# Performance work log

Hardware: AMD Instinct MI355X
Metric: run time of the kernel (lower is better)

The kernel has to match this reference:

```python
import jax, jax.numpy as jnp
import numpy as np

N_USERS = 50000
N_ENTITIES = 100000
N_NODES = N_USERS + N_ENTITIES
N_EDGES = 3000000
EMB_DIM = 64
WEIGHT_SIZES = [64, 64, 32, 16]  # [emb_dim] + weight_size
BATCH = 8192
LEAKY_SLOPE = 0.2  # KGAT (TF reference) uses leaky_relu alpha=0.2
EPS = 1e-12


def setup_inputs() -> dict:
    key = jax.random.key(0)
    ks = jax.random.split(key, 24)
    inp = {}
    inp["users"] = jax.random.randint(ks[0], (BATCH,), 0, N_USERS, dtype=jnp.int32)
    inp["pos_items"] = jax.random.randint(ks[1], (BATCH,), 0, N_ENTITIES, dtype=jnp.int32)
    inp["neg_items"] = jax.random.randint(ks[2], (BATCH,), 0, N_ENTITIES, dtype=jnp.int32)
    inp["all_h"] = jax.random.randint(ks[3], (N_EDGES,), 0, N_NODES, dtype=jnp.int32)
    inp["all_t"] = jax.random.randint(ks[4], (N_EDGES,), 0, N_NODES, dtype=jnp.int32)
    inp["A_values"] = jax.random.uniform(ks[5], (N_EDGES,), dtype=jnp.float32)
    inp["user_embed"] = jax.random.normal(ks[6], (N_USERS, EMB_DIM), dtype=jnp.float32) * 0.1
    inp["entity_embed"] = jax.random.normal(ks[7], (N_ENTITIES, EMB_DIM), dtype=jnp.float32) * 0.1
    ki = 8
    for k in range(3):
        din, dout = WEIGHT_SIZES[k], WEIGHT_SIZES[k + 1]
        scale = float(np.sqrt(2.0 / (din + dout)))  # xavier-ish
        inp[f"W_gc_{k}"] = jax.random.normal(ks[ki], (din, dout), dtype=jnp.float32) * scale; ki += 1
        inp[f"b_gc_{k}"] = jax.random.normal(ks[ki], (1, dout), dtype=jnp.float32) * scale; ki += 1
        inp[f"W_bi_{k}"] = jax.random.normal(ks[ki], (din, dout), dtype=jnp.float32) * scale; ki += 1
        inp[f"b_bi_{k}"] = jax.random.normal(ks[ki], (1, dout), dtype=jnp.float32) * scale; ki += 1
    return inp


def _bi_interaction(ego, all_h, all_t, A_values, layers, n_nodes):
    # KGAT bi-interaction aggregator over edge-list sparse adjacency.
    outs = [ego]
    for (W_gc, b_gc, W_bi, b_bi) in layers:
        # sparse A @ ego : gather tails, weight by attention, scatter-add to heads
        msgs = A_values[:, None] * ego[all_t]                       # [E, d]
        side = jax.ops.segment_sum(msgs, all_h, num_segments=n_nodes)  # [N, d]
        sum_emb = jax.nn.leaky_relu((ego + side) @ W_gc + b_gc, negative_slope=LEAKY_SLOPE)
        bi_emb = jax.nn.leaky_relu((ego * side) @ W_bi + b_bi, negative_slope=LEAKY_SLOPE)
        ego = sum_emb + bi_emb
        norm = ego / jnp.maximum(jnp.linalg.norm(ego, axis=1, keepdims=True), EPS)
        outs.append(norm)
    return jnp.concatenate(outs, axis=1)  # [N, 64+64+32+16]


def reference(users, pos_items, neg_items, all_h, all_t, A_values,
              user_embed, entity_embed,
              W_gc_0, b_gc_0, W_bi_0, b_bi_0,
              W_gc_1, b_gc_1, W_bi_1, b_bi_1,
              W_gc_2, b_gc_2, W_bi_2, b_bi_2):
    n_users = user_embed.shape[0]
    n_nodes = n_users + entity_embed.shape[0]
    ego = jnp.concatenate([user_embed, entity_embed], axis=0)  # [N, 64]
    layers = [(W_gc_0, b_gc_0, W_bi_0, b_bi_0),
              (W_gc_1, b_gc_1, W_bi_1, b_bi_1),
              (W_gc_2, b_gc_2, W_bi_2, b_bi_2)]
    all_emb = _bi_interaction(ego, all_h, all_t, A_values, layers, n_nodes)
    ua, ea = all_emb[:n_users], all_emb[n_users:]
    u_e = ua[users]
    pos_i_e = ea[pos_items]
    neg_i_e = ea[neg_items]
    return (u_e, pos_i_e, neg_i_e)
```

## Files before the change

### kernel.cpp

```cpp
#include <hip/hip_runtime.h>
#include <math.h>

#define N_USERS    50000
#define N_ENTITIES 100000
#define N_NODES    150000
#define N_EDGES    3000000
#define BATCH      8192
#define SLOPE      0.2f
#define EPSF       1e-12f

#define NBUK   2344
#define CAP    1536
#define STR    2560
#define PADM   16
#define BLK_E  12288
#define NPB    ((N_EDGES + BLK_E - 1) / BLK_E)
#define PBLK   1024
#define EPT    (BLK_E / PBLK)
#define CH     4096
#define GC_STRIDE 16
#define CASTB  ((N_NODES * 64 / 4 + PBLK - 1) / PBLK)

__device__ __forceinline__ unsigned f2bf(float f) {
    unsigned u = __float_as_uint(f);
    return (u + 0x7FFFu + ((u >> 16) & 1u)) >> 16;
}
__device__ __forceinline__ float bf_lo(unsigned d) { return __uint_as_float(d << 16); }
__device__ __forceinline__ float bf_hi(unsigned d) { return __uint_as_float(d); }

__global__ __launch_bounds__(PBLK)
void prep_k(const int* __restrict__ all_h, const int* __restrict__ all_t,
            const float* __restrict__ A,
            int* __restrict__ gcursor, int2* __restrict__ rec,
            const float* __restrict__ user_emb, const float* __restrict__ ent_emb,
            unsigned short* __restrict__ ego0_bf) {
    __shared__ int pos[NBUK];
    __shared__ int gofs[NBUK];
    __shared__ int wsum[PBLK / 64];
    __shared__ int2 srec[CH];
    __shared__ int  sdst[CH];

    int t = threadIdx.x;

    if (blockIdx.x >= NPB) {
        int idx = (blockIdx.x - NPB) * PBLK + t;
        const int total = N_NODES * 64 / 4;
        if (idx >= total) return;
        int ge = idx * 4;
        const float* src = (ge < N_USERS * 64) ? user_emb + ge
                                               : ent_emb + (ge - N_USERS * 64);
        float4 v = *(const float4*)src;
        ushort4 o;
        o.x = (unsigned short)f2bf(v.x);
        o.y = (unsigned short)f2bf(v.y);
        o.z = (unsigned short)f2bf(v.z);
        o.w = (unsigned short)f2bf(v.w);
        *(ushort4*)(ego0_bf + ge) = o;
        return;
    }

    for (int i = t; i < NBUK; i += PBLK) pos[i] = 0;
    __syncthreads();

    int e0 = blockIdx.x * BLK_E;
    int e1 = e0 + BLK_E; if (e1 > N_EDGES) e1 = N_EDGES;
    int tot = e1 - e0;

    int h[EPT]; int tt[EPT]; float aa[EPT];
    #pragma unroll
    for (int k = 0; k < EPT; ++k) {
        int e = e0 + k * PBLK + t;
        bool v = e < e1;
        h[k]  = v ? all_h[e] : -1;
        tt[k] = v ? all_t[e] : 0;
        aa[k] = v ? A[e] : 0.f;
    }
    #pragma unroll
    for (int k = 0; k < EPT; ++k)
        if (h[k] >= 0) atomicAdd(&pos[h[k] >> 6], 1);
    __syncthreads();

    int c[3], g[3];
    int i0 = t * 3;
    int tsum = 0;
    #pragma unroll
    for (int j = 0; j < 3; ++j) {
        int idx = i0 + j;
        c[j] = (idx < NBUK) ? pos[idx] : 0;
        tsum += c[j];
        g[j] = (idx < NBUK && c[j]) ? atomicAdd(&gcursor[idx * GC_STRIDE], c[j]) : 0;
    }

    int lane = t & 63, w = t >> 6;
    int incl = tsum;
    #pragma unroll
    for (int off = 1; off < 64; off <<= 1) {
        int x = __shfl_up(incl, off, 64);
        if (lane >= off) incl += x;
    }
    if (lane == 63) wsum[w] = incl;
    __syncthreads();
    int wbase = 0;
    for (int j = 0; j < w; ++j) wbase += wsum[j];
    int excl = wbase + (incl - tsum);

    #pragma unroll
    for (int j = 0; j < 3; ++j) {
        int idx = i0 + j;
        if (idx < NBUK) { pos[idx] = excl; gofs[idx] = g[j] - excl; }
        excl += c[j];
    }
    __syncthreads();

    int pp[EPT], gd[EPT];
    #pragma unroll
    for (int k = 0; k < EPT; ++k) {
        if (h[k] >= 0) {
            int b = h[k] >> 6;
            int p = atomicAdd(&pos[b], 1);
            pp[k] = p;
            int gr = gofs[b] + p;
            gd[k] = (gr < CAP) ? b * STR + gr : -1;
        } else {
            pp[k] = -1; gd[k] = -1;
        }
    }

    for (int base = 0; base < tot; base += CH) {
        __syncthreads();
        int lim = tot - base; if (lim > CH) lim = CH;
        #pragma unroll
        for (int k = 0; k < EPT; ++k) {
            int s = pp[k] - base;
            if (s >= 0 && s < CH) {
                srec[s] = make_int2(tt[k] | ((h[k] & 63) << 18), __float_as_int(aa[k]));
                sdst[s] = gd[k];
            }
        }
        __syncthreads();
        for (int s = t; s < lim; s += PBLK) {
            int d = sdst[s];
            if (d >= 0) rec[d] = srec[s];
        }
    }
}

__global__ __launch_bounds__(256)
void local_sort_k(const int* __restrict__ gcursor, int2* __restrict__ rec,
                  int2* __restrict__ range) {
    __shared__ int2 sin[CAP];
    __shared__ int2 sout[STR];
    __shared__ int cnt64[64];
    __shared__ int pos64[64];
    __shared__ int s_ptot;
    int b = blockIdx.x, t = threadIdx.x;
    int cnt = gcursor[(size_t)b * GC_STRIDE]; if (cnt > CAP) cnt = CAP;

    if (t < 64) cnt64[t] = 0;
    __syncthreads();

    for (int i = t; i < cnt; i += 256) {
        int2 p = rec[(size_t)b * STR + i];
        sin[i] = p;
        atomicAdd(&cnt64[(p.x >> 18) & 63], 1);
    }
    __syncthreads();

    if (t < 64) {
        int v = cnt64[t];
        int pv = (v + PADM - 1) & ~(PADM - 1);
        int sum = pv;
        #pragma unroll
        for (int off = 1; off < 64; off <<= 1) {
            int x = __shfl_up(sum, off, 64);
            if (t >= off) sum += x;
        }
        pos64[t] = sum - pv;
        if (t == 63) s_ptot = sum;
    }
    __syncthreads();
    int ptot = s_ptot;

    for (int i = t; i < ptot; i += 256) sout[i] = make_int2(0, 0);
    __syncthreads();

    for (int i = t; i < cnt; i += 256) {
        int2 p = sin[i];
        int l = (p.x >> 18) & 63;
        int dst = atomicAdd(&pos64[l], 1);
        sout[dst] = make_int2(p.x & 0x3FFFF, p.y);
    }
    __syncthreads();

    for (int i = t; i < ptot; i += 256)
        rec[(size_t)b * STR + i] = sout[i];

    if (t < 64) {
        int v = cnt64[t];
        int pv = (v + PADM - 1) & ~(PADM - 1);
        int sum = pv;
        #pragma unroll
        for (int off = 1; off < 64; off <<= 1) {
            int x = __shfl_up(sum, off, 64);
            if (t >= off) sum += x;
        }
        int start = b * STR + (sum - pv);
        int node = b * 64 + t;
        if (node < N_NODES) range[node] = make_int2(start, start + pv);
    }
}

template<int DIN>
__global__ __launch_bounds__(256)
void side_k(const int2* __restrict__ range, const int2* __restrict__ rec,
            const unsigned short* __restrict__ tab, float* __restrict__ side) {
    constexpr int LPR = DIN / 8;
    constexpr int EPW = 64 / LPR;

    int w = threadIdx.x >> 6;
    int lane = threadIdx.x & 63;
    int h = blockIdx.x * 4 + w;

    int2 rg = range[h];
    int e0 = rg.x, e1 = rg.y;
    int g = lane / LPR;
    int q = lane % LPR;

    float acc[8];
    #pragma unroll
    for (int j = 0; j < 8; ++j) acc[j] = 0.f;

    int e = e0;
    for (; e + 2 * EPW <= e1; e += 2 * EPW) {
        int2 p0 = rec[e + g];
        int2 p1 = rec[e + EPW + g];
        float a0 = __int_as_float(p0.y);
        float a1 = __int_as_float(p1.y);
        uint4 d0 = *(const uint4*)(tab + (unsigned)(p0.x * DIN) + q * 8);
        uint4 d1 = *(const uint4*)(tab + (unsigned)(p1.x * DIN) + q * 8);
        acc[0] = fmaf(a0, bf_lo(d0.x), acc[0]);
        acc[1] = fmaf(a0, bf_hi(d0.x), acc[1]);
        acc[2] = fmaf(a0, bf_lo(d0.y), acc[2]);
        acc[3] = fmaf(a0, bf_hi(d0.y), acc[3]);
        acc[4] = fmaf(a0, bf_lo(d0.z), acc[4]);
        acc[5] = fmaf(a0, bf_hi(d0.z), acc[5]);
        acc[6] = fmaf(a0, bf_lo(d0.w), acc[6]);
        acc[7] = fmaf(a0, bf_hi(d0.w), acc[7]);
        acc[0] = fmaf(a1, bf_lo(d1.x), acc[0]);
        acc[1] = fmaf(a1, bf_hi(d1.x), acc[1]);
        acc[2] = fmaf(a1, bf_lo(d1.y), acc[2]);
        acc[3] = fmaf(a1, bf_hi(d1.y), acc[3]);
        acc[4] = fmaf(a1, bf_lo(d1.z), acc[4]);
        acc[5] = fmaf(a1, bf_hi(d1.z), acc[5]);
        acc[6] = fmaf(a1, bf_lo(d1.w), acc[6]);
        acc[7] = fmaf(a1, bf_hi(d1.w), acc[7]);
    }
    if (e < e1) {
        int2 p0 = rec[e + g];
        float a0 = __int_as_float(p0.y);
        uint4 d0 = *(const uint4*)(tab + (unsigned)(p0.x * DIN) + q * 8);
        acc[0] = fmaf(a0, bf_lo(d0.x), acc[0]);
        acc[1] = fmaf(a0, bf_hi(d0.x), acc[1]);
        acc[2] = fmaf(a0, bf_lo(d0.y), acc[2]);
        acc[3] = fmaf(a0, bf_hi(d0.y), acc[3]);
        acc[4] = fmaf(a0, bf_lo(d0.z), acc[4]);
        acc[5] = fmaf(a0, bf_hi(d0.z), acc[5]);
        acc[6] = fmaf(a0, bf_lo(d0.w), acc[6]);
        acc[7] = fmaf(a0, bf_hi(d0.w), acc[7]);
    }

    #pragma unroll
    for (int off = LPR; off < 64; off <<= 1)
        #pragma unroll
        for (int j = 0; j < 8; ++j) acc[j] += __shfl_xor(acc[j], off, 64);

    if (lane < LPR) {
        float* dst = side + (size_t)h * DIN + q * 8;
        *(float4*)dst       = make_float4(acc[0], acc[1], acc[2], acc[3]);
        *(float4*)(dst + 4) = make_float4(acc[4], acc[5], acc[6], acc[7]);
    }
}

template<int DIN, int DOUT, int TILE_ROWS, bool CONCAT, bool OUT_BF>
__global__ __launch_bounds__(256)
void transform_k(const unsigned short* __restrict__ ego_in,
                 const float* __restrict__ user_emb, const float* __restrict__ ent_emb,
                 const float* __restrict__ side,
                 const float* __restrict__ Wgc, const float* __restrict__ bgc,
                 const float* __restrict__ Wbi, const float* __restrict__ bbi,
                 void* __restrict__ ego_out) {
    constexpr int NG = DOUT / 8;
    constexpr int RG = 256 / NG;
    constexpr int RT = TILE_ROWS / RG;
    constexpr int STRIDE = DIN + 4;
    constexpr int KC8 = DIN / 8;

    __shared__ float sWgc[DIN * DOUT], sWbi[DIN * DOUT];
    __shared__ float sU[TILE_ROWS * STRIDE], sV[TILE_ROWS * STRIDE];

    int t = threadIdx.x;

    for (int i = t * 4; i < DIN * DOUT; i += 1024) {
        *(float4*)&sWgc[i] = *(const float4*)&Wgc[i];
        *(float4*)&sWbi[i] = *(const float4*)&Wbi[i];
    }

    int base = blockIdx.x * TILE_ROWS;
    for (int f = t; f < TILE_ROWS * KC8; f += 256) {
        int row = f / KC8, c8 = f % KC8;
        int n = base + row;
        int nc = n < N_NODES ? n : N_NODES - 1;
        float ev[8];
        if (CONCAT) {
            const float* erow = (nc < N_USERS) ? user_emb + (size_t)nc * 64
                                               : ent_emb + (size_t)(nc - N_USERS) * 64;
            float4 a = *(const float4*)(erow + c8 * 8);
            float4 b = *(const float4*)(erow + c8 * 8 + 4);
            ev[0] = a.x; ev[1] = a.y; ev[2] = a.z; ev[3] = a.w;
            ev[4] = b.x; ev[5] = b.y; ev[6] = b.z; ev[7] = b.w;
        } else {
            uint4 d = *(const uint4*)(ego_in + (size_t)nc * DIN + c8 * 8);
            ev[0] = bf_lo(d.x); ev[1] = bf_hi(d.x);
            ev[2] = bf_lo(d.y); ev[3] = bf_hi(d.y);
            ev[4] = bf_lo(d.z); ev[5] = bf_hi(d.z);
            ev[6] = bf_lo(d.w); ev[7] = bf_hi(d.w);
        }
        const float* srow = side + (size_t)nc * DIN + c8 * 8;
        float4 s0 = *(const float4*)srow;
        float4 s1 = *(const float4*)(srow + 4);
        float sv8[8] = {s0.x, s0.y, s0.z, s0.w, s1.x, s1.y, s1.z, s1.w};
        float* pu = &sU[row * STRIDE + c8 * 8];
        float* pv = &sV[row * STRIDE + c8 * 8];
        *(float4*)pu       = make_float4(ev[0] + sv8[0], ev[1] + sv8[1], ev[2] + sv8[2], ev[3] + sv8[3]);
        *(float4*)(pu + 4) = make_float4(ev[4] + sv8[4], ev[5] + sv8[5], ev[6] + sv8[6], ev[7] + sv8[7]);
        *(float4*)pv       = make_float4(ev[0] * sv8[0], ev[1] * sv8[1], ev[2] * sv8[2], ev[3] * sv8[3]);
        *(float4*)(pv + 4) = make_float4(ev[4] * sv8[4], ev[5] * sv8[5], ev[6] * sv8[6], ev[7] * sv8[7]);
    }
    __syncthreads();

    int cg = t % NG, rgi = t / NG;
    int c0 = cg * 8;
    int r0 = rgi * RT;

    float accg[RT][8], accb[RT][8];
    #pragma unroll
    for (int r = 0; r < RT; ++r)
        #pragma unroll
        for (int j = 0; j < 8; ++j) { accg[r][j] = 0.f; accb[r][j] = 0.f; }

    for (int k = 0; k < DIN; k += 4) {
        float4 u4[RT], v4[RT];
        #pragma unroll
        for (int r = 0; r < RT; ++r) {
            u4[r] = *(const float4*)&sU[(r0 + r) * STRIDE + k];
            v4[r] = *(const float4*)&sV[(r0 + r) * STRIDE + k];
        }
        #pragma unroll
        for (int kk = 0; kk < 4; ++kk) {
            float4 wg0 = *(const float4*)&sWgc[(k + kk) * DOUT + c0];
            float4 wg1 = *(const float4*)&sWgc[(k + kk) * DOUT + c0 + 4];
            float4 wb0 = *(const float4*)&sWbi[(k + kk) * DOUT + c0];
            float4 wb1 = *(const float4*)&sWbi[(k + kk) * DOUT + c0 + 4];
            #pragma unroll
            for (int r = 0; r < RT; ++r) {
                float u = ((const float*)&u4[r])[kk];
                float v = ((const float*)&v4[r])[kk];
                accg[r][0] = fmaf(u, wg0.x, accg[r][0]);
                accg[r][1] = fmaf(u, wg0.y, accg[r][1]);
                accg[r][2] = fmaf(u, wg0.z, accg[r][2]);
                accg[r][3] = fmaf(u, wg0.w, accg[r][3]);
                accg[r][4] = fmaf(u, wg1.x, accg[r][4]);
                accg[r][5] = fmaf(u, wg1.y, accg[r][5]);
                accg[r][6] = fmaf(u, wg1.z, accg[r][6]);
                accg[r][7] = fmaf(u, wg1.w, accg[r][7]);
                accb[r][0] = fmaf(v, wb0.x, accb[r][0]);
                accb[r][1] = fmaf(v, wb0.y, accb[r][1]);
                accb[r][2] = fmaf(v, wb0.z, accb[r][2]);
                accb[r][3] = fmaf(v, wb0.w, accb[r][3]);
                accb[r][4] = fmaf(v, wb1.x, accb[r][4]);
                accb[r][5] = fmaf(v, wb1.y, accb[r][5]);
                accb[r][6] = fmaf(v, wb1.z, accb[r][6]);
                accb[r][7] = fmaf(v, wb1.w, accb[r][7]);
            }
        }
    }

    float4 bg0 = *(const float4*)&bgc[c0];
    float4 bg1 = *(const float4*)&bgc[c0 + 4];
    float4 bb0 = *(const float4*)&bbi[c0];
    float4 bb1 = *(const float4*)&bbi[c0 + 4];
    float bg[8] = {bg0.x, bg0.y, bg0.z, bg0.w, bg1.x, bg1.y, bg1.z, bg1.w};
    float bb[8] = {bb0.x, bb0.y, bb0.z, bb0.w, bb1.x, bb1.y, bb1.z, bb1.w};

    #pragma unroll
    for (int r = 0; r < RT; ++r) {
        int n = base + r0 + r;
        if (n < N_NODES) {
            float o[8];
            #pragma unroll
            for (int j = 0; j < 8; ++j) {
                float gg = accg[r][j] + bg[j];
                float b2 = accb[r][j] + bb[j];
                gg = gg > 0.f ? gg : SLOPE * gg;
                b2 = b2 > 0.f ? b2 : SLOPE * b2;
                o[j] = gg + b2;
            }
            if (OUT_BF) {
                unsigned short* dst = (unsigned short*)ego_out + (size_t)n * DOUT + c0;
                uint4 wv;
                wv.x = f2bf(o[0]) | (f2bf(o[1]) << 16);
                wv.y = f2bf(o[2]) | (f2bf(o[3]) << 16);
                wv.z = f2bf(o[4]) | (f2bf(o[5]) << 16);
                wv.w = f2bf(o[6]) | (f2bf(o[7]) << 16);
                *(uint4*)dst = wv;
            } else {
                float* dst = (float*)ego_out + (size_t)n * DOUT + c0;
                *(float4*)dst       = make_float4(o[0], o[1], o[2], o[3]);
                *(float4*)(dst + 4) = make_float4(o[4], o[5], o[6], o[7]);
            }
        }
    }
}

__global__ __launch_bounds__(256)
void gather_k(const int* __restrict__ users, const int* __restrict__ pos,
              const int* __restrict__ neg,
              const float* __restrict__ user_emb, const float* __restrict__ ent_emb,
              const unsigned short* __restrict__ ego1_bf,
              const unsigned short* __restrict__ ego2_bf,
              const float* __restrict__ ego3,
              float* __restrict__ out) {
    int w = threadIdx.x >> 6;
    int lane = threadIdx.x & 63;
    int r = blockIdx.x * 4 + w;
    int which = r / BATCH;
    int i = r - which * BATCH;
    int node;
    if (which == 0)      node = users[i];
    else if (which == 1) node = N_USERS + pos[i];
    else                 node = N_USERS + neg[i];

    float* o = out + (size_t)r * 176;

    float x0 = (node < N_USERS) ? user_emb[(size_t)node * 64 + lane]
                                : ent_emb[(size_t)(node - N_USERS) * 64 + lane];
    o[lane] = x0;

    float x1 = __uint_as_float((unsigned)ego1_bf[(size_t)node * 64 + lane] << 16);
    float ss = x1 * x1;
    #pragma unroll
    for (int off = 32; off > 0; off >>= 1) ss += __shfl_xor(ss, off, 64);
    o[64 + lane] = x1 / fmaxf(sqrtf(ss), EPSF);

    float x2 = (lane < 32)
        ? __uint_as_float((unsigned)ego2_bf[(size_t)node * 32 + lane] << 16) : 0.f;
    float ss2 = x2 * x2;
    #pragma unroll
    for (int off = 32; off > 0; off >>= 1) ss2 += __shfl_xor(ss2, off, 64);
    if (lane < 32) o[128 + lane] = x2 / fmaxf(sqrtf(ss2), EPSF);

    float x3 = (lane < 16) ? ego3[(size_t)node * 16 + lane] : 0.f;
    float ss3 = x3 * x3;
    #pragma unroll
    for (int off = 32; off > 0; off >>= 1) ss3 += __shfl_xor(ss3, off, 64);
    if (lane < 16) o[160 + lane] = x3 / fmaxf(sqrtf(ss3), EPSF);
}

extern "C" void kernel_launch(void* const* d_in, const int* in_sizes, int n_in,
                              void* d_out, int out_size, void* d_ws, size_t ws_size,
                              hipStream_t stream) {
    const int*   users    = (const int*)d_in[0];
    const int*   pos      = (const int*)d_in[1];
    const int*   neg      = (const int*)d_in[2];
    const int*   all_h    = (const int*)d_in[3];
    const int*   all_t    = (const int*)d_in[4];
    const float* A        = (const float*)d_in[5];
    const float* user_emb = (const float*)d_in[6];
    const float* ent_emb  = (const float*)d_in[7];
    const float* Wgc0 = (const float*)d_in[8];
    const float* bgc0 = (const float*)d_in[9];
    const float* Wbi0 = (const float*)d_in[10];
    const float* bbi0 = (const float*)d_in[11];
    const float* Wgc1 = (const float*)d_in[12];
    const float* bgc1 = (const float*)d_in[13];
    const float* Wbi1 = (const float*)d_in[14];
    const float* bbi1 = (const float*)d_in[15];
    const float* Wgc2 = (const float*)d_in[16];
    const float* bgc2 = (const float*)d_in[17];
    const float* Wbi2 = (const float*)d_in[18];
    const float* bbi2 = (const float*)d_in[19];

    char* p = (char*)d_ws;
    int*   gcursor = (int*)p;            p += ((size_t)NBUK * GC_STRIDE * 4 + 255) & ~255ull;
    int2*  rec     = (int2*)p;           char* rec_base = p;
    p += ((size_t)NBUK * STR * 8 + 255) & ~255ull;
    int2*  range   = (int2*)p;           p += ((size_t)N_NODES * 8 + 255) & ~255ull;
    float* side    = (float*)p;          p += ((size_t)N_NODES * 64 * 4 + 255) & ~255ull;
    unsigned short* ego0_bf = (unsigned short*)p; p += ((size_t)N_NODES * 64 * 2 + 255) & ~255ull;
    unsigned short* ego1_bf = (unsigned short*)p; p += ((size_t)N_NODES * 64 * 2 + 255) & ~255ull;
    unsigned short* ego2_bf = (unsigned short*)p; p += ((size_t)N_NODES * 32 * 2 + 255) & ~255ull;
    float* ego3    = (float*)rec_base;
    float* out     = (float*)d_out;

    const int nodeBlocks = N_NODES / 4;

    (void)hipMemsetAsync(gcursor, 0, (size_t)NBUK * GC_STRIDE * 4, stream);
    prep_k<<<NPB + CASTB, PBLK, 0, stream>>>(all_h, all_t, A, gcursor, rec,
                                             user_emb, ent_emb, ego0_bf);
    local_sort_k<<<NBUK, 256, 0, stream>>>(gcursor, rec, range);

    side_k<64><<<nodeBlocks, 256, 0, stream>>>(range, rec, ego0_bf, side);
    transform_k<64, 64, 64, true, true><<<(N_NODES + 63) / 64, 256, 0, stream>>>(
        nullptr, user_emb, ent_emb, side, Wgc0, bgc0, Wbi0, bbi0, ego1_bf);

    side_k<64><<<nodeBlocks, 256, 0, stream>>>(range, rec, ego1_bf, side);
    transform_k<64, 32, 64, false, true><<<(N_NODES + 63) / 64, 256, 0, stream>>>(
        ego1_bf, nullptr, nullptr, side, Wgc1, bgc1, Wbi1, bbi1, ego2_bf);

    side_k<32><<<nodeBlocks, 256, 0, stream>>>(range, rec, ego2_bf, side);
    transform_k<32, 16, 128, false, false><<<(N_NODES + 127) / 128, 256, 0, stream>>>(
        ego2_bf, nullptr, nullptr, side, Wgc2, bgc2, Wbi2, bbi2, ego3);

    gather_k<<<3 * BATCH / 4, 256, 0, stream>>>(
        users, pos, neg, user_emb, ent_emb, ego1_bf, ego2_bf, ego3, out);
}
```

Baseline: 487.7 us.

## Replace global atomic bucket cursors with per-block prefix table and contiguous writes

```diff
diff --git a/kernel.cpp b/kernel.cpp
--- a/kernel.cpp
+++ b/kernel.cpp
@@ -18,7 +18,7 @@
 #define PBLK   1024
 #define EPT    (BLK_E / PBLK)
 #define CH     4096
-#define GC_STRIDE 16
+#define PFW    (NBUK + 1)
 #define CASTB  ((N_NODES * 64 / 4 + PBLK - 1) / PBLK)
 
 __device__ __forceinline__ unsigned f2bf(float f) {
@@ -31,14 +31,12 @@
 __global__ __launch_bounds__(PBLK)
 void prep_k(const int* __restrict__ all_h, const int* __restrict__ all_t,
             const float* __restrict__ A,
-            int* __restrict__ gcursor, int2* __restrict__ rec,
+            int* __restrict__ prefix, int2* __restrict__ rec_src,
             const float* __restrict__ user_emb, const float* __restrict__ ent_emb,
             unsigned short* __restrict__ ego0_bf) {
     __shared__ int pos[NBUK];
-    __shared__ int gofs[NBUK];
     __shared__ int wsum[PBLK / 64];
     __shared__ int2 srec[CH];
-    __shared__ int  sdst[CH];
 
     int t = threadIdx.x;
 
@@ -80,7 +78,7 @@
         if (h[k] >= 0) atomicAdd(&pos[h[k] >> 6], 1);
     __syncthreads();
 
-    int c[3], g[3];
+    int c[3];
     int i0 = t * 3;
     int tsum = 0;
     #pragma unroll
@@ -88,7 +86,6 @@
         int idx = i0 + j;
         c[j] = (idx < NBUK) ? pos[idx] : 0;
         tsum += c[j];
-        g[j] = (idx < NBUK && c[j]) ? atomicAdd(&gcursor[idx * GC_STRIDE], c[j]) : 0;
     }
 
     int lane = t & 63, w = t >> 6;
@@ -104,27 +101,20 @@
     for (int j = 0; j < w; ++j) wbase += wsum[j];
     int excl = wbase + (incl - tsum);
 
+    size_t prow = (size_t)blockIdx.x * PFW;
     #pragma unroll
     for (int j = 0; j < 3; ++j) {
         int idx = i0 + j;
-        if (idx < NBUK) { pos[idx] = excl; gofs[idx] = g[j] - excl; }
+        if (idx < NBUK) { pos[idx] = excl; prefix[prow + idx] = excl; }
         excl += c[j];
     }
-    __syncthreads();
-
-    int pp[EPT], gd[EPT];
-    #pragma unroll
-    for (int k = 0; k < EPT; ++k) {
-        if (h[k] >= 0) {
-            int b = h[k] >> 6;
-            int p = atomicAdd(&pos[b], 1);
-            pp[k] = p;
-            int gr = gofs[b] + p;
-            gd[k] = (gr < CAP) ? b * STR + gr : -1;
-        } else {
-            pp[k] = -1; gd[k] = -1;
-        }
-    }
+    if (t == PBLK - 1) prefix[prow + NBUK] = excl;
+    __syncthreads();
+
+    int pp[EPT];
+    #pragma unroll
+    for (int k = 0; k < EPT; ++k)
+        pp[k] = (h[k] >= 0) ? atomicAdd(&pos[h[k] >> 6], 1) : -1;
 
     for (int base = 0; base < tot; base += CH) {
         __syncthreads();
@@ -132,37 +122,59 @@
         #pragma unroll
         for (int k = 0; k < EPT; ++k) {
             int s = pp[k] - base;
-            if (s >= 0 && s < CH) {
+            if (s >= 0 && s < CH)
                 srec[s] = make_int2(tt[k] | ((h[k] & 63) << 18), __float_as_int(aa[k]));
-                sdst[s] = gd[k];
-            }
         }
         __syncthreads();
-        for (int s = t; s < lim; s += PBLK) {
-            int d = sdst[s];
-            if (d >= 0) rec[d] = srec[s];
-        }
+        const int4* s4 = (const int4*)srec;
+        int4* d4 = (int4*)(rec_src + e0 + base);
+        int lim2 = lim >> 1;
+        for (int s = t; s < lim2; s += PBLK) d4[s] = s4[s];
     }
 }
 
 __global__ __launch_bounds__(256)
-void local_sort_k(const int* __restrict__ gcursor, int2* __restrict__ rec,
-                  int2* __restrict__ range) {
+void local_sort_k(const int* __restrict__ prefix, const int2* __restrict__ rec_src,
+                  int2* __restrict__ rec, int2* __restrict__ range) {
     __shared__ int2 sin[CAP];
     __shared__ int2 sout[STR];
     __shared__ int cnt64[64];
     __shared__ int pos64[64];
+    __shared__ int sc[256];
     __shared__ int s_ptot;
     int b = blockIdx.x, t = threadIdx.x;
-    int cnt = gcursor[(size_t)b * GC_STRIDE]; if (cnt > CAP) cnt = CAP;
 
     if (t < 64) cnt64[t] = 0;
-    __syncthreads();
-
-    for (int i = t; i < cnt; i += 256) {
-        int2 p = rec[(size_t)b * STR + i];
-        sin[i] = p;
-        atomicAdd(&cnt64[(p.x >> 18) & 63], 1);
+
+    int rstart = 0, n_t = 0;
+    if (t < NPB) {
+        const int* prow = prefix + (size_t)t * PFW + b;
+        int s0 = prow[0];
+        int s1 = prow[1];
+        rstart = t * BLK_E + s0;
+        n_t = s1 - s0;
+    }
+    sc[t] = n_t;
+    __syncthreads();
+
+    for (int off = 1; off < 256; off <<= 1) {
+        int v = sc[t];
+        int u = (t >= off) ? sc[t - off] : 0;
+        __syncthreads();
+        sc[t] = v + u;
+        __syncthreads();
+    }
+    int cnt = sc[255]; if (cnt > CAP) cnt = CAP;
+
+    if (t < NPB && n_t > 0) {
+        int d = sc[t] - n_t;
+        for (int j = 0; j < n_t; ++j) {
+            int dj = d + j;
+            if (dj >= CAP) break;
+            int2 p = rec_src[rstart + j];
+            sin[dj] = p;
+            atomicAdd(&cnt64[(p.x >> 18) & 63], 1);
+        }
     }
     __syncthreads();
 
@@ -491,11 +503,12 @@
     const float* bbi2 = (const float*)d_in[19];
 
     char* p = (char*)d_ws;
-    int*   gcursor = (int*)p;            p += ((size_t)NBUK * GC_STRIDE * 4 + 255) & ~255ull;
+    int*   prefix  = (int*)p;            p += ((size_t)NPB * PFW * 4 + 255) & ~255ull;
+    float* side    = (float*)p;
+    int2*  rec_src = (int2*)p;           p += ((size_t)N_NODES * 64 * 4 + 255) & ~255ull;
     int2*  rec     = (int2*)p;           char* rec_base = p;
     p += ((size_t)NBUK * STR * 8 + 255) & ~255ull;
     int2*  range   = (int2*)p;           p += ((size_t)N_NODES * 8 + 255) & ~255ull;
-    float* side    = (float*)p;          p += ((size_t)N_NODES * 64 * 4 + 255) & ~255ull;
     unsigned short* ego0_bf = (unsigned short*)p; p += ((size_t)N_NODES * 64 * 2 + 255) & ~255ull;
     unsigned short* ego1_bf = (unsigned short*)p; p += ((size_t)N_NODES * 64 * 2 + 255) & ~255ull;
     unsigned short* ego2_bf = (unsigned short*)p; p += ((size_t)N_NODES * 32 * 2 + 255) & ~255ull;
@@ -504,10 +517,9 @@
 
     const int nodeBlocks = N_NODES / 4;
 
-    (void)hipMemsetAsync(gcursor, 0, (size_t)NBUK * GC_STRIDE * 4, stream);
-    prep_k<<<NPB + CASTB, PBLK, 0, stream>>>(all_h, all_t, A, gcursor, rec,
+    prep_k<<<NPB + CASTB, PBLK, 0, stream>>>(all_h, all_t, A, prefix, rec_src,
                                              user_emb, ent_emb, ego0_bf);
-    local_sort_k<<<NBUK, 256, 0, stream>>>(gcursor, rec, range);
+    local_sort_k<<<NBUK, 256, 0, stream>>>(prefix, rec_src, rec, range);
 
     side_k<64><<<nodeBlocks, 256, 0, stream>>>(range, rec, ego0_bf, side);
     transform_k<64, 64, 64, true, true><<<(N_NODES + 63) / 64, 256, 0, stream>>>(
```

Measured after the change: 476.6 us. 1.02x faster.
